# Optimization experiments

Hardware: AMD Instinct MI355X
Metric: run time of the kernel (lower is better)

Reference implementation:

```python
import jax, jax.numpy as jnp
import numpy as np

VOCAB, CTX, EMBED, HEADS = 32000, 2048, 1024, 16


def setup_inputs() -> dict:
    key = jax.random.key(0)
    ks = jax.random.split(key, 10)
    E = EMBED
    s = 0.02
    return {
        "x": jax.random.randint(ks[0], (2, 2048), 0, VOCAB, dtype=jnp.int32),
        "tok_emb": jax.random.normal(ks[1], (VOCAB, E), jnp.float32) * s,
        "pos_emb": jax.random.normal(ks[2], (CTX, E), jnp.float32) * s,
        "qkv_w": jax.random.normal(ks[3], (E, 3 * E), jnp.float32) * s,
        "qkv_b": jnp.zeros((3 * E,), jnp.float32),
        "proj_w": jax.random.normal(ks[4], (E, E), jnp.float32) * s,
        "proj_b": jnp.zeros((E,), jnp.float32),
        "fc_w": jax.random.normal(ks[5], (E, VOCAB), jnp.float32) * s,
        "fc_b": jnp.zeros((VOCAB,), jnp.float32),
    }


def reference(x, tok_emb, pos_emb, qkv_w, qkv_b, proj_w, proj_b, fc_w, fc_b):
    B, T = x.shape
    H = HEADS
    E = tok_emb.shape[1]
    hd = E // H
    h = tok_emb[x] + pos_emb[:T][None, :, :]                      # [B,T,E]
    qkv = h @ qkv_w + qkv_b                                       # [B,T,3E]
    q, k, v = jnp.split(qkv, 3, axis=-1)
    # [B,T,E] -> [B,H,T,hd]
    q = q.reshape(B, T, H, hd).transpose(0, 2, 1, 3)
    k = k.reshape(B, T, H, hd).transpose(0, 2, 1, 3)
    v = v.reshape(B, T, H, hd).transpose(0, 2, 1, 3)
    att = jnp.einsum("bhqd,bhkd->bhqk", q, k) / jnp.sqrt(jnp.float32(hd))
    causal = jnp.tril(jnp.ones((T, T), dtype=bool))
    att = jnp.where(causal[None, None], att, jnp.float32(-jnp.inf))
    att = jax.nn.softmax(att, axis=-1)
    out = jnp.einsum("bhqk,bhkd->bhqd", att, v)                   # [B,H,T,hd]
    out = out.transpose(0, 2, 1, 3).reshape(B, T, E)
    out = out @ proj_w + proj_b
    return out @ fc_w + fc_b                                      # [B,T,VOCAB]
```

## Files before the change

### kernel.cpp

```cpp
#include <hip/hip_runtime.h>

#define BATCH 2
#define T 2048
#define E 1024
#define NH 16
#define HD 64
#define M (BATCH*T)
#define K3 (3*E)
#define VOCAB 32000

typedef __attribute__((ext_vector_type(8))) short s16x8;
typedef __attribute__((ext_vector_type(4))) short s16x4;
typedef __attribute__((ext_vector_type(4))) float f32x4;

__device__ inline unsigned short f2bf(float f) {
  union { float f; unsigned u; } x; x.f = f;
  unsigned r = x.u + 0x7fffu + ((x.u >> 16) & 1u);
  return (unsigned short)(r >> 16);
}

__device__ inline void gload16(const void* g, void* l) {
  __builtin_amdgcn_global_load_lds(
      (const __attribute__((address_space(1))) unsigned int*)g,
      (__attribute__((address_space(3))) unsigned int*)l, 16, 0, 0);
}

__device__ inline void wt_body(const float* __restrict__ W,
    unsigned short* __restrict__ Wt, int N, int n0, int k0, int t,
    float (*tile)[65]) {
  int kl = t >> 2, c = t & 3;
  #pragma unroll
  for (int i = 0; i < 4; i++) {
    float4 v4 = *(const float4*)(W + (size_t)(k0 + kl) * N + n0 + c * 16 + i * 4);
    tile[kl][c * 16 + i * 4 + 0] = v4.x;
    tile[kl][c * 16 + i * 4 + 1] = v4.y;
    tile[kl][c * 16 + i * 4 + 2] = v4.z;
    tile[kl][c * 16 + i * 4 + 3] = v4.w;
  }
  __syncthreads();
  #pragma unroll
  for (int j = 0; j < 2; j++) {
    int idx = t + j * 256;
    int nl = idx >> 3, kq = (idx & 7) * 8;
    s16x8 o;
    #pragma unroll
    for (int i = 0; i < 8; i++) o[i] = (short)f2bf(tile[kq + i][nl]);
    *(s16x8*)(Wt + (size_t)(n0 + nl) * 1024 + k0 + kq) = o;
  }
}

__global__ __launch_bounds__(256) void k_pre(const int* __restrict__ x,
    const float* __restrict__ tok, const float* __restrict__ pos,
    unsigned short* __restrict__ hb,
    const float* __restrict__ qkvw, unsigned short* __restrict__ qkvwt,
    const float* __restrict__ projw, unsigned short* __restrict__ projwt) {
  __shared__ __align__(16) float tile[64][65];
  int gid = blockIdx.x, t = threadIdx.x;
  if (gid < 4096) {
    int row = gid;
    int tt = row & (T - 1);
    int tokid = x[row];
    float4 a = ((const float4*)(tok + (size_t)tokid * E))[t];
    float4 p = ((const float4*)(pos + (size_t)tt * E))[t];
    s16x4 o;
    o[0] = (short)f2bf(a.x + p.x); o[1] = (short)f2bf(a.y + p.y);
    o[2] = (short)f2bf(a.z + p.z); o[3] = (short)f2bf(a.w + p.w);
    *(s16x4*)(hb + (size_t)row * E + t * 4) = o;
    return;
  }
  if (gid < 4864) {
    int idx = gid - 4096;
    wt_body(qkvw, qkvwt, K3, (idx % 48) * 64, (idx / 48) * 64, t, tile);
    return;
  }
  int idx = gid - 4864;
  wt_body(projw, projwt, E, (idx % 16) * 64, (idx / 16) * 64, t, tile);
}

template<int MODE>
__global__ __launch_bounds__(256) void k_bgemm(
    const unsigned short* __restrict__ A, const unsigned short* __restrict__ Bt,
    const float* __restrict__ bias, float* __restrict__ C, int N,
    unsigned short* __restrict__ qo, unsigned short* __restrict__ ko,
    unsigned short* __restrict__ vo, unsigned short* __restrict__ Cb) {
  __shared__ char lds[16384];
  char* As = lds;
  char* Bs = lds + 8192;
  int tid = threadIdx.x;
  int lane = tid & 63;
  int wv = tid >> 6;
  int wm = wv >> 1, wn = wv & 1;
  int n0 = blockIdx.x * 128, m0 = blockIdx.y * 128;
  int fr = lane & 15, fq = lane >> 4;

  f32x4 acc[4][4];
  #pragma unroll
  for (int i = 0; i < 4; i++)
    #pragma unroll
    for (int j = 0; j < 4; j++) acc[i][j] = (f32x4){0.f, 0.f, 0.f, 0.f};

  int p0 = tid * 16, p1 = tid * 16 + 4096;
  int r0 = p0 >> 6, c0 = p0 & 63;
  int r1 = p1 >> 6, c1 = p1 & 63;
  int cs0 = c0 ^ (((r0 >> 1) & 3) << 4);
  int cs1 = c1 ^ (((r1 >> 1) & 3) << 4);
  const char* ga0 = (const char*)(A + (size_t)(m0 + r0) * 1024) + cs0;
  const char* ga1 = (const char*)(A + (size_t)(m0 + r1) * 1024) + cs1;
  const char* gb0 = (const char*)(Bt + (size_t)(n0 + r0) * 1024) + cs0;
  const char* gb1 = (const char*)(Bt + (size_t)(n0 + r1) * 1024) + cs1;

  int aoff[4], boff[4];
  #pragma unroll
  for (int i = 0; i < 4; i++) {
    int ra = wm * 64 + i * 16 + fr;
    aoff[i] = ra * 64 + ((fq * 16) ^ (((ra >> 1) & 3) << 4));
    int rb = wn * 64 + i * 16 + fr;
    boff[i] = rb * 64 + ((fq * 16) ^ (((rb >> 1) & 3) << 4));
  }

  for (int kb = 0; kb < 2048; kb += 64) {
    gload16(ga0 + kb, As + p0);
    gload16(ga1 + kb, As + p1);
    gload16(gb0 + kb, Bs + p0);
    gload16(gb1 + kb, Bs + p1);
    __syncthreads();
    s16x8 af[4], bfr[4];
    #pragma unroll
    for (int i = 0; i < 4; i++) af[i] = *(const s16x8*)(As + aoff[i]);
    #pragma unroll
    for (int i = 0; i < 4; i++) bfr[i] = *(const s16x8*)(Bs + boff[i]);
    #pragma unroll
    for (int mi = 0; mi < 4; mi++)
      #pragma unroll
      for (int ni = 0; ni < 4; ni++)
        acc[mi][ni] = __builtin_amdgcn_mfma_f32_16x16x32_bf16(
            af[mi], bfr[ni], acc[mi][ni], 0, 0, 0);
    __syncthreads();
  }

  if (MODE == 1) {
    #pragma unroll
    for (int mi = 0; mi < 4; mi++) {
      #pragma unroll
      for (int ni = 0; ni < 4; ni++) {
        int n = n0 + wn * 64 + ni * 16 + fr;
        int which = n >> 10;
        int e = n & (E - 1);
        int hh = e >> 6, d = e & 63;
        int mb = m0 + wm * 64 + mi * 16 + fq * 4;
        int b = mb >> 11, tt0 = mb & (T - 1);
        float bv = bias[n];
        if (which == 2) {
          s16x4 pk;
          #pragma unroll
          for (int j = 0; j < 4; j++) pk[j] = (short)f2bf(acc[mi][ni][j] + bv);
          *(s16x4*)(vo + ((size_t)(b * NH + hh) * 64 + d) * T + tt0) = pk;
        } else {
          unsigned short* dst = (which == 0) ? qo : ko;
          #pragma unroll
          for (int j = 0; j < 4; j++)
            dst[((size_t)(b * NH + hh) * T + tt0 + j) * 64 + d] =
                f2bf(acc[mi][ni][j] + bv);
        }
      }
    }
  } else {
    #pragma unroll
    for (int mi = 0; mi < 4; mi++) {
      #pragma unroll
      for (int ni = 0; ni < 4; ni++) {
        #pragma unroll
        for (int j = 0; j < 4; j++) {
          int m = m0 + wm * 64 + mi * 16 + fq * 4 + j;
          int n = n0 + wn * 64 + ni * 16 + fr;
          float val = acc[mi][ni][j] + bias[n];
          if (MODE == 0) C[(size_t)m * N + n] = val;
          else           Cb[(size_t)m * 1024 + n] = f2bf(val);
        }
      }
    }
  }
}

__global__ __launch_bounds__(512, 2) void k_fc(
    const unsigned short* __restrict__ A, const unsigned short* __restrict__ Bt,
    const float* __restrict__ bias, float* __restrict__ C) {
  __shared__ __align__(16) char lds[131072];
  int tid = threadIdx.x, lane = tid & 63, wv = tid >> 6;
  int WM = wv >> 2, WN = wv & 3;
  int fr = lane & 15, fq = lane >> 4;

  int bid = blockIdx.x;
  int wg = (bid & 7) * 250 + (bid >> 3);
  int m0 = (wg & 15) * 256;
  int n0 = (wg >> 4) * 256;

  const char* gA[4]; const char* gB[4]; int lo[4];
  #pragma unroll
  for (int j = 0; j < 4; j++) {
    int i = tid + j * 512;
    int r = i >> 3, c = i & 7;
    int cc = c ^ (r & 7);
    gA[j] = (const char*)A + ((size_t)(m0 + r) * 1024 + cc * 8) * 2;
    gB[j] = (const char*)Bt + ((size_t)(n0 + r) * 1024 + cc * 8) * 2;
    lo[j] = i * 16;
  }

  f32x4 acc[8][4];
  #pragma unroll
  for (int i = 0; i < 8; i++)
    #pragma unroll
    for (int j = 0; j < 4; j++) acc[i][j] = (f32x4){0.f, 0.f, 0.f, 0.f};

  #pragma unroll
  for (int j = 0; j < 4; j++) {
    gload16(gA[j], lds + lo[j]);
    gload16(gB[j], lds + 65536 + lo[j]);
  }
  __syncthreads();

  for (int t = 0; t < 16; t++) {
    int cur = t & 1;
    if (t + 1 < 16) {
      int kb = (t + 1) * 128;
      int nxt = cur ^ 1;
      #pragma unroll
      for (int j = 0; j < 4; j++) {
        gload16(gA[j] + kb, lds + nxt * 32768 + lo[j]);
        gload16(gB[j] + kb, lds + 65536 + nxt * 32768 + lo[j]);
      }
    }
    const char* As = lds + cur * 32768;
    const char* Bs = lds + 65536 + cur * 32768;
    #pragma unroll
    for (int kh = 0; kh < 2; kh++) {
      s16x8 af[8], bf[4];
      #pragma unroll
      for (int mi = 0; mi < 8; mi++) {
        int r = WM * 128 + mi * 16 + fr;
        af[mi] = *(const s16x8*)(As + r * 128 + (((kh * 4 + fq) ^ (r & 7)) << 4));
      }
      #pragma unroll
      for (int ni = 0; ni < 4; ni++) {
        int r = WN * 64 + ni * 16 + fr;
        bf[ni] = *(const s16x8*)(Bs + r * 128 + (((kh * 4 + fq) ^ (r & 7)) << 4));
      }
      __builtin_amdgcn_s_setprio(1);
      #pragma unroll
      for (int mi = 0; mi < 8; mi++)
        #pragma unroll
        for (int ni = 0; ni < 4; ni++)
          acc[mi][ni] = __builtin_amdgcn_mfma_f32_16x16x32_bf16(
              af[mi], bf[ni], acc[mi][ni], 0, 0, 0);
      __builtin_amdgcn_s_setprio(0);
    }
    __syncthreads();
  }

  #pragma unroll
  for (int mi = 0; mi < 8; mi++) {
    #pragma unroll
    for (int ni = 0; ni < 4; ni++) {
      int n = n0 + WN * 64 + ni * 16 + fr;
      float bv = bias[n];
      #pragma unroll
      for (int j = 0; j < 4; j++) {
        int m = m0 + WM * 128 + mi * 16 + fq * 4 + j;
        C[(size_t)m * VOCAB + n] = acc[mi][ni][j] + bv;
      }
    }
  }
}

#define BM 128
#define BN 128
#define BKF 32
#define LDT (BM + 4)
__global__ __launch_bounds__(256) void k_gemm32(
    const float* __restrict__ A, const float* __restrict__ Bw,
    const float* __restrict__ bias, float* __restrict__ C, int N) {
  __shared__ float As[BKF * LDT];
  __shared__ float Bs[BKF * LDT];
  int tid = threadIdx.x;
  int tx = tid & 15, ty = tid >> 4;
  int n0 = blockIdx.x * BN;
  int m0 = blockIdx.y * BM;
  float acc[8][8];
  #pragma unroll
  for (int i = 0; i < 8; i++)
    #pragma unroll
    for (int j = 0; j < 8; j++) acc[i][j] = 0.f;
  for (int k0 = 0; k0 < E; k0 += BKF) {
    #pragma unroll
    for (int i = 0; i < 4; i++) {
      int f = i * 256 + tid;
      int ml = f >> 3, c4 = f & 7;
      float4 va = *(const float4*)(A + (size_t)(m0 + ml) * E + k0 + c4 * 4);
      As[(c4 * 4 + 0) * LDT + ml] = va.x;
      As[(c4 * 4 + 1) * LDT + ml] = va.y;
      As[(c4 * 4 + 2) * LDT + ml] = va.z;
      As[(c4 * 4 + 3) * LDT + ml] = va.w;
    }
    #pragma unroll
    for (int i = 0; i < 4; i++) {
      int f = i * 256 + tid;
      int kk = f >> 5, c4 = f & 31;
      float4 vb = *(const float4*)(Bw + (size_t)(k0 + kk) * N + n0 + c4 * 4);
      *(float4*)(Bs + kk * LDT + c4 * 4) = vb;
    }
    __syncthreads();
    #pragma unroll
    for (int kk = 0; kk < BKF; kk++) {
      const float4* ar = (const float4*)(As + kk * LDT);
      const float4* br = (const float4*)(Bs + kk * LDT);
      float4 a0 = ar[ty * 2], a1 = ar[ty * 2 + 1];
      float4 b0 = br[tx * 2], b1 = br[tx * 2 + 1];
      float av[8] = {a0.x, a0.y, a0.z, a0.w, a1.x, a1.y, a1.z, a1.w};
      float bvv[8] = {b0.x, b0.y, b0.z, b0.w, b1.x, b1.y, b1.z, b1.w};
      #pragma unroll
      for (int i = 0; i < 8; i++)
        #pragma unroll
        for (int j = 0; j < 8; j++)
          acc[i][j] = fmaf(av[i], bvv[j], acc[i][j]);
    }
    __syncthreads();
  }
  int mbase = m0 + ty * 8;
  int nbase = n0 + tx * 8;
  #pragma unroll
  for (int i = 0; i < 8; i++) {
    float* crow = C + (size_t)(mbase + i) * N + nbase;
    #pragma unroll
    for (int j = 0; j < 8; j++) crow[j] = acc[i][j] + bias[nbase + j];
  }
}

__global__ __launch_bounds__(256) void k_attn_wt(
    const unsigned short* __restrict__ qb, const unsigned short* __restrict__ kb,
    const unsigned short* __restrict__ vtb, unsigned short* __restrict__ o,
    const float* __restrict__ fcw, unsigned short* __restrict__ fcwt) {
  __shared__ __align__(16) char lds[40960];
  int gid = blockIdx.x;
  int tid = threadIdx.x;

  if (gid >= 512) {
    int idx = gid - 512;
    wt_body(fcw, fcwt, VOCAB, (idx % 500) * 64, (idx / 500) * 64, tid,
            (float(*)[65])lds);
    return;
  }

  int qt = 15 - (gid >> 5);
  int bh = gid & 31;
  int b = bh >> 4, hh = bh & 15;
  int lane = tid & 63, wv = tid >> 6;
  int fr = lane & 15, fq = lane >> 4;
  int q0 = qt * 128;
  int qw0 = q0 + wv * 32;
  const char* Kg = (const char*)(kb + (size_t)bh * T * 64);
  const char* Vg = (const char*)(vtb + (size_t)bh * 64 * T);
  char* Pl = lds + 32768 + wv * 2048;

  s16x8 qf[2][2];
  #pragma unroll
  for (int g = 0; g < 2; g++) {
    const unsigned short* Qg = qb + ((size_t)bh * T + qw0 + g * 16) * 64;
    qf[g][0] = *(const s16x8*)(Qg + (size_t)fr * 64 + fq * 8);
    qf[g][1] = *(const s16x8*)(Qg + (size_t)fr * 64 + 32 + fq * 8);
  }

  f32x4 po[2][4];
  float mrow[2][4], lrow[2][4];
  #pragma unroll
  for (int g = 0; g < 2; g++)
    #pragma unroll
    for (int j = 0; j < 4; j++) {
      po[g][j] = (f32x4){0.f, 0.f, 0.f, 0.f};
      mrow[g][j] = -1e30f; lrow[g][j] = 0.f;
    }

  int ntiles = qt * 2 + 2;
  int i0 = tid, i1 = tid + 256;
  int sr0 = i0 >> 3, sc0 = ((i0 & 7) ^ (sr0 & 7)) << 4;
  int sr1 = i1 >> 3, sc1 = ((i1 & 7) ^ (sr1 & 7)) << 4;

  {
    gload16(Kg + (size_t)sr0 * 128 + sc0, lds + i0 * 16);
    gload16(Kg + (size_t)sr1 * 128 + sc1, lds + i1 * 16);
    gload16(Vg + (size_t)sr0 * (T * 2) + sc0, lds + 16384 + i0 * 16);
    gload16(Vg + (size_t)sr1 * (T * 2) + sc1, lds + 16384 + i1 * 16);
  }
  __syncthreads();
  int cur = 0;

  for (int kt = 0; kt < ntiles; kt++) {
    int kv0 = kt * 64;
    if (kt + 1 < ntiles) {
      size_t kvn = (size_t)(kv0 + 64);
      char* kd = lds + (cur ^ 1) * 8192;
      char* vd = lds + 16384 + (cur ^ 1) * 8192;
      gload16(Kg + (kvn + sr0) * 128 + sc0, kd + i0 * 16);
      gload16(Kg + (kvn + sr1) * 128 + sc1, kd + i1 * 16);
      gload16(Vg + (size_t)sr0 * (T * 2) + kvn * 2 + sc0, vd + i0 * 16);
      gload16(Vg + (size_t)sr1 * (T * 2) + kvn * 2 + sc1, vd + i1 * 16);
    }
    const char* Kt = lds + cur * 8192;
    const char* Vt = lds + 16384 + cur * 8192;

    #pragma unroll
    for (int g = 0; g < 2; g++) {
      int qw = qw0 + g * 16;
      f32x4 s[4];
      #pragma unroll
      for (int ni = 0; ni < 4; ni++) {
        s[ni] = (f32x4){0.f, 0.f, 0.f, 0.f};
        int r = ni * 16 + fr;
        s16x8 kf0 = *(const s16x8*)(Kt + r * 128 + ((fq ^ (r & 7)) << 4));
        s16x8 kf1 = *(const s16x8*)(Kt + r * 128 + (((4 + fq) ^ (r & 7)) << 4));
        s[ni] = __builtin_amdgcn_mfma_f32_16x16x32_bf16(qf[g][0], kf0, s[ni], 0, 0, 0);
        s[ni] = __builtin_amdgcn_mfma_f32_16x16x32_bf16(qf[g][1], kf1, s[ni], 0, 0, 0);
      }

      bool needm = (kv0 + 63 > qw);
      #pragma unroll
      for (int jj = 0; jj < 4; jj++) {
        int row = qw + fq * 4 + jj;
        float tm = -1e30f;
        #pragma unroll
        for (int ni = 0; ni < 4; ni++) {
          float val = s[ni][jj] * 0.125f;
          if (needm) { int col = kv0 + ni * 16 + fr; if (col > row) val = -1e30f; }
          s[ni][jj] = val;
          tm = fmaxf(tm, val);
        }
        #pragma unroll
        for (int mk = 1; mk < 16; mk <<= 1) tm = fmaxf(tm, __shfl_xor(tm, mk));
        if (__any(tm > mrow[g][jj] + 8.f)) {
          float nm = fmaxf(mrow[g][jj], tm);
          float corr = __expf(mrow[g][jj] - nm);
          mrow[g][jj] = nm;
          #pragma unroll
          for (int ni = 0; ni < 4; ni++) po[g][ni][jj] *= corr;
          lrow[g][jj] *= corr;
        }
        float mref = mrow[g][jj];
        float rs = 0.f;
        #pragma unroll
        for (int ni = 0; ni < 4; ni++) {
          float pv = __expf(s[ni][jj] - mref);
          s[ni][jj] = pv;
          rs += pv;
        }
        #pragma unroll
        for (int mk = 1; mk < 16; mk <<= 1) rs += __shfl_xor(rs, mk);
        lrow[g][jj] += rs;
      }

      asm volatile("s_waitcnt lgkmcnt(0)" ::: "memory");
      #pragma unroll
      for (int ni = 0; ni < 4; ni++) {
        int col = ni * 16 + fr;
        #pragma unroll
        for (int jj = 0; jj < 4; jj++) {
          int qq = fq * 4 + jj;
          *(unsigned short*)(Pl + qq * 128 + (((col >> 3) ^ (qq & 7)) << 4) +
                             (col & 7) * 2) = f2bf(s[ni][jj]);
        }
      }
      asm volatile("s_waitcnt lgkmcnt(0)" ::: "memory");

      s16x8 pa0 = *(const s16x8*)(Pl + fr * 128 + ((fq ^ (fr & 7)) << 4));
      s16x8 pa1 = *(const s16x8*)(Pl + fr * 128 + (((4 + fq) ^ (fr & 7)) << 4));
      #pragma unroll
      for (int ni = 0; ni < 4; ni++) {
        int r = ni * 16 + fr;
        s16x8 vf0 = *(const s16x8*)(Vt + r * 128 + ((fq ^ (r & 7)) << 4));
        s16x8 vf1 = *(const s16x8*)(Vt + r * 128 + (((4 + fq) ^ (r & 7)) << 4));
        po[g][ni] = __builtin_amdgcn_mfma_f32_16x16x32_bf16(pa0, vf0, po[g][ni], 0, 0, 0);
        po[g][ni] = __builtin_amdgcn_mfma_f32_16x16x32_bf16(pa1, vf1, po[g][ni], 0, 0, 0);
      }
    }
    __syncthreads();
    cur ^= 1;
  }

  #pragma unroll
  for (int g = 0; g < 2; g++)
    #pragma unroll
    for (int jj = 0; jj < 4; jj++) {
      float inv = 1.f / lrow[g][jj];
      int row = qw0 + g * 16 + fq * 4 + jj;
      unsigned short* orow = o + ((size_t)(b * T + row)) * E + hh * 64;
      #pragma unroll
      for (int ni = 0; ni < 4; ni++)
        orow[ni * 16 + fr] = f2bf(po[g][ni][jj] * inv);
    }
}

extern "C" void kernel_launch(void* const* d_in, const int* in_sizes, int n_in,
                              void* d_out, int out_size, void* d_ws, size_t ws_size,
                              hipStream_t stream) {
  const int*   x      = (const int*)d_in[0];
  const float* tok    = (const float*)d_in[1];
  const float* pos    = (const float*)d_in[2];
  const float* qkv_w  = (const float*)d_in[3];
  const float* qkv_b  = (const float*)d_in[4];
  const float* proj_w = (const float*)d_in[5];
  const float* proj_b = (const float*)d_in[6];
  const float* fc_w   = (const float*)d_in[7];
  const float* fc_b   = (const float*)d_in[8];
  float* out = (float*)d_out;
  float* ws  = (float*)d_ws;

  unsigned short* hb      = (unsigned short*)out;
  unsigned short* qkv_wt  = (unsigned short*)(out + 2097152);
  unsigned short* qbuf    = (unsigned short*)(out + 3670016);
  unsigned short* kbuf    = (unsigned short*)(out + 5767168);
  unsigned short* vtbuf   = (unsigned short*)(out + 7864320);
  unsigned short* aob     = (unsigned short*)(out + 9961472);
  unsigned short* proj_wt = (unsigned short*)(out + 12058624);

  const size_t WS_FAST = (size_t)(2097152 + 16384000) * 4;

  k_pre<<<5120, 256, 0, stream>>>(x, tok, pos, hb, qkv_w, qkv_wt, proj_w, proj_wt);
  k_bgemm<1><<<dim3(K3 / 128, M / 128), 256, 0, stream>>>(
      hb, qkv_wt, qkv_b, nullptr, K3, qbuf, kbuf, vtbuf, nullptr);

  if (ws_size >= WS_FAST) {
    unsigned short* h2b   = (unsigned short*)ws;
    unsigned short* fc_wt = (unsigned short*)(ws + 2097152);
    k_attn_wt<<<8512, 256, 0, stream>>>(qbuf, kbuf, vtbuf, aob, fc_w, fc_wt);
    k_bgemm<2><<<dim3(E / 128, M / 128), 256, 0, stream>>>(
        aob, proj_wt, proj_b, nullptr, E, nullptr, nullptr, nullptr, h2b);
    k_fc<<<dim3((M / 256) * (VOCAB / 256)), 512, 0, stream>>>(
        h2b, fc_wt, fc_b, out);
  } else {
    float* h2 = ws;
    k_attn_wt<<<512, 256, 0, stream>>>(qbuf, kbuf, vtbuf, aob, nullptr, nullptr);
    k_bgemm<0><<<dim3(E / 128, M / 128), 256, 0, stream>>>(
        aob, proj_wt, proj_b, h2, E, nullptr, nullptr, nullptr, nullptr);
    k_gemm32<<<dim3(VOCAB / BN, M / BM), 256, 0, stream>>>(
        h2, fc_w, fc_b, out, VOCAB);
  }
}
```

Baseline: 522.2 us.

## Restructure FC GEMM main loop into four barrier-separated MFMA phases with prefetch depth two

The vocab-projection GEMM loop is rewritten as a ping-pong schedule. Each K-step is split into four quadrant phases separated by s_barrier, with setprio raised around the MFMA clusters and LDS fragment reads interleaved between phases. Global-to-LDS loads now run two K-steps ahead instead of one, and explicit vmcnt waits replace __syncthreads. The aim is to overlap memory and LDS traffic with MFMA issue across the two resident waves per SIMD, at the cost of more barriers and a more fragile hand schedule.

Measured after the change: 546.8 us. +4.7%, slower.

```diff
diff --git a/kernel.cpp b/kernel.cpp
--- a/kernel.cpp
+++ b/kernel.cpp
@@ -195,16 +195,24 @@
   int m0 = (wg & 15) * 256;
   int n0 = (wg >> 4) * 256;
 
-  const char* gA[4]; const char* gB[4]; int lo[4];
-  #pragma unroll
-  for (int j = 0; j < 4; j++) {
-    int i = tid + j * 512;
-    int r = i >> 3, c = i & 7;
-    int cc = c ^ (r & 7);
-    gA[j] = (const char*)A + ((size_t)(m0 + r) * 1024 + cc * 8) * 2;
-    gB[j] = (const char*)Bt + ((size_t)(n0 + r) * 1024 + cc * 8) * 2;
-    lo[j] = i * 16;
-  }
+  int c0 = tid, c1 = tid + 512;
+  int sr0 = c0 >> 3, sc0 = ((c0 & 7) ^ (sr0 & 7)) * 16;
+  int sr1 = c1 >> 3, sc1 = ((c1 & 7) ^ (sr1 & 7)) * 16;
+  int sl0 = c0 * 16, sl1 = c1 * 16;
+
+#define STAGE_A(t,h) do { char* d_ = lds + ((t) & 1) * 65536 + (h) * 16384;          \
+    gload16((const char*)A + (size_t)(m0 + (h)*128 + sr0) * 2048 + (t)*128 + sc0, d_ + sl0); \
+    gload16((const char*)A + (size_t)(m0 + (h)*128 + sr1) * 2048 + (t)*128 + sc1, d_ + sl1); \
+  } while (0)
+#define STAGE_B(t,h) do { char* d_ = lds + ((t) & 1) * 65536 + 32768 + (h) * 16384;  \
+    gload16((const char*)Bt + (size_t)(n0 + (h)*128 + sr0) * 2048 + (t)*128 + sc0, d_ + sl0); \
+    gload16((const char*)Bt + (size_t)(n0 + (h)*128 + sr1) * 2048 + (t)*128 + sc1, d_ + sl1); \
+  } while (0)
+#define PHASE_IN do { __builtin_amdgcn_sched_barrier(0); __builtin_amdgcn_s_barrier(); \
+    asm volatile("s_waitcnt lgkmcnt(0)" ::: "memory");                                 \
+    __builtin_amdgcn_sched_barrier(0); __builtin_amdgcn_s_setprio(1); } while (0)
+#define PHASE_OUT do { __builtin_amdgcn_s_setprio(0); __builtin_amdgcn_sched_barrier(0); \
+    __builtin_amdgcn_s_barrier(); __builtin_amdgcn_sched_barrier(0); } while (0)
 
   f32x4 acc[8][4];
   #pragma unroll
@@ -212,50 +220,103 @@
     #pragma unroll
     for (int j = 0; j < 4; j++) acc[i][j] = (f32x4){0.f, 0.f, 0.f, 0.f};
 
-  #pragma unroll
-  for (int j = 0; j < 4; j++) {
-    gload16(gA[j], lds + lo[j]);
-    gload16(gB[j], lds + 65536 + lo[j]);
-  }
-  __syncthreads();
+  STAGE_A(0, 0); STAGE_A(0, 1); STAGE_B(0, 0); STAGE_B(0, 1);
+  STAGE_A(1, 0); STAGE_A(1, 1); STAGE_B(1, 0); STAGE_B(1, 1);
+  asm volatile("s_waitcnt vmcnt(8)" ::: "memory");
+  __builtin_amdgcn_sched_barrier(0);
+  __builtin_amdgcn_s_barrier();
+  __builtin_amdgcn_sched_barrier(0);
 
   for (int t = 0; t < 16; t++) {
-    int cur = t & 1;
-    if (t + 1 < 16) {
-      int kb = (t + 1) * 128;
-      int nxt = cur ^ 1;
-      #pragma unroll
-      for (int j = 0; j < 4; j++) {
-        gload16(gA[j] + kb, lds + nxt * 32768 + lo[j]);
-        gload16(gB[j] + kb, lds + 65536 + nxt * 32768 + lo[j]);
-      }
-    }
-    const char* As = lds + cur * 32768;
-    const char* Bs = lds + 65536 + cur * 32768;
-    #pragma unroll
-    for (int kh = 0; kh < 2; kh++) {
-      s16x8 af[8], bf[4];
-      #pragma unroll
-      for (int mi = 0; mi < 8; mi++) {
-        int r = WM * 128 + mi * 16 + fr;
-        af[mi] = *(const s16x8*)(As + r * 128 + (((kh * 4 + fq) ^ (r & 7)) << 4));
-      }
-      #pragma unroll
-      for (int ni = 0; ni < 4; ni++) {
-        int r = WN * 64 + ni * 16 + fr;
-        bf[ni] = *(const s16x8*)(Bs + r * 128 + (((kh * 4 + fq) ^ (r & 7)) << 4));
-      }
-      __builtin_amdgcn_s_setprio(1);
-      #pragma unroll
-      for (int mi = 0; mi < 8; mi++)
-        #pragma unroll
-        for (int ni = 0; ni < 4; ni++)
+    const char* Ah = lds + (t & 1) * 65536 + WM * 16384;
+    const char* Bh = lds + (t & 1) * 65536 + 32768 + (WN >> 1) * 16384;
+    int clB = (WN & 1) * 64;
+    s16x8 af[4][2], bf[4][2];
+
+    #pragma unroll
+    for (int mi = 0; mi < 4; mi++) {
+      int rl = mi * 16 + fr;
+      #pragma unroll
+      for (int ks = 0; ks < 2; ks++)
+        af[mi][ks] = *(const s16x8*)(Ah + rl * 128 + (((ks * 4 + fq) ^ (rl & 7)) << 4));
+    }
+    #pragma unroll
+    for (int ni = 0; ni < 2; ni++) {
+      int cl = clB + ni * 16 + fr;
+      #pragma unroll
+      for (int ks = 0; ks < 2; ks++)
+        bf[ni][ks] = *(const s16x8*)(Bh + cl * 128 + (((ks * 4 + fq) ^ (cl & 7)) << 4));
+    }
+    PHASE_IN;
+    #pragma unroll
+    for (int mi = 0; mi < 4; mi++)
+      #pragma unroll
+      for (int ni = 0; ni < 2; ni++)
+        #pragma unroll
+        for (int ks = 0; ks < 2; ks++)
           acc[mi][ni] = __builtin_amdgcn_mfma_f32_16x16x32_bf16(
-              af[mi], bf[ni], acc[mi][ni], 0, 0, 0);
-      __builtin_amdgcn_s_setprio(0);
-    }
-    __syncthreads();
-  }
+              af[mi][ks], bf[ni][ks], acc[mi][ni], 0, 0, 0);
+    PHASE_OUT;
+
+    #pragma unroll
+    for (int ni = 2; ni < 4; ni++) {
+      int cl = clB + ni * 16 + fr;
+      #pragma unroll
+      for (int ks = 0; ks < 2; ks++)
+        bf[ni][ks] = *(const s16x8*)(Bh + cl * 128 + (((ks * 4 + fq) ^ (cl & 7)) << 4));
+    }
+    PHASE_IN;
+    #pragma unroll
+    for (int mi = 0; mi < 4; mi++)
+      #pragma unroll
+      for (int ni = 2; ni < 4; ni++)
+        #pragma unroll
+        for (int ks = 0; ks < 2; ks++)
+          acc[mi][ni] = __builtin_amdgcn_mfma_f32_16x16x32_bf16(
+              af[mi][ks], bf[ni][ks], acc[mi][ni], 0, 0, 0);
+    PHASE_OUT;
+
+    #pragma unroll
+    for (int mi = 0; mi < 4; mi++) {
+      int rl = (mi + 4) * 16 + fr;
+      #pragma unroll
+      for (int ks = 0; ks < 2; ks++)
+        af[mi][ks] = *(const s16x8*)(Ah + rl * 128 + (((ks * 4 + fq) ^ (rl & 7)) << 4));
+    }
+    if (t + 2 < 16) { STAGE_B(t + 2, 0); STAGE_B(t + 2, 1); }
+    PHASE_IN;
+    #pragma unroll
+    for (int mi = 0; mi < 4; mi++)
+      #pragma unroll
+      for (int ni = 2; ni < 4; ni++)
+        #pragma unroll
+        for (int ks = 0; ks < 2; ks++)
+          acc[mi + 4][ni] = __builtin_amdgcn_mfma_f32_16x16x32_bf16(
+              af[mi][ks], bf[ni][ks], acc[mi + 4][ni], 0, 0, 0);
+    PHASE_OUT;
+
+    if (t + 2 < 16) { STAGE_A(t + 2, 0); STAGE_A(t + 2, 1); }
+    PHASE_IN;
+    #pragma unroll
+    for (int mi = 0; mi < 4; mi++)
+      #pragma unroll
+      for (int ni = 0; ni < 2; ni++)
+        #pragma unroll
+        for (int ks = 0; ks < 2; ks++)
+          acc[mi + 4][ni] = __builtin_amdgcn_mfma_f32_16x16x32_bf16(
+              af[mi][ks], bf[ni][ks], acc[mi + 4][ni], 0, 0, 0);
+    __builtin_amdgcn_s_setprio(0);
+    __builtin_amdgcn_sched_barrier(0);
+    if (t < 14)       asm volatile("s_waitcnt vmcnt(8)" ::: "memory");
+    else if (t == 14) asm volatile("s_waitcnt vmcnt(0)" ::: "memory");
+    __builtin_amdgcn_sched_barrier(0);
+    __builtin_amdgcn_s_barrier();
+    __builtin_amdgcn_sched_barrier(0);
+  }
+#undef STAGE_A
+#undef STAGE_B
+#undef PHASE_IN
+#undef PHASE_OUT
 
   #pragma unroll
   for (int mi = 0; mi < 8; mi++) {
```
